# Optimization experiments

Measured on AMD Instinct MI355X. Metric: run time of the kernel, lower is better.

## Reference

```python
import jax, jax.numpy as jnp
import numpy as np

DIM = 1024
B, K = 8192, 16


def setup_inputs() -> dict:
    key = jax.random.key(0)
    ks = jax.random.split(key, 7)
    # xavier_uniform bound for square [C,C]: sqrt(6/(C+C))
    bq = float(np.sqrt(6.0 / (DIM + DIM)))
    ba_bound = float(np.sqrt(6.0 / (DIM + 1)))
    return {
        "query": jax.random.normal(ks[0], (B, DIM), dtype=jnp.float32),
        "key": jax.random.normal(ks[1], (B, K, DIM), dtype=jnp.float32),
        "value": jax.random.normal(ks[2], (B, K, DIM), dtype=jnp.float32),
        "Wq": jax.random.uniform(ks[3], (DIM, DIM), jnp.float32, -bq, bq),
        "Wk": jax.random.uniform(ks[4], (DIM, DIM), jnp.float32, -bq, bq),
        "Wa": jax.random.uniform(ks[5], (1, DIM), jnp.float32, -ba_bound, ba_bound),
        "ba": jnp.ones((1,), dtype=jnp.float32),
    }


def reference(query, key, value, Wq, Wk, Wa, ba):
    # query: [B, C]; key/value: [B, K, C]
    C = query.shape[-1]
    res = query
    q = query[:, None, :]                       # [B, 1, C]
    k = jnp.concatenate([q, key], axis=1)       # [B, K+1, C] (query prepended)
    v = jnp.concatenate([q, value], axis=1)     # [B, K+1, C]
    qp = q @ Wq.T                               # [B, 1, C]
    kp = k @ Wk.T                               # [B, K+1, C]
    scale = 1.0 / jnp.sqrt(jnp.asarray(C, dtype=jnp.float32))
    scores = jnp.einsum('bqc,bkc->bqk', qp, kp) * scale   # [B, 1, K+1]
    attn_w = jax.nn.softmax(scores, axis=-1)
    attn = jnp.einsum('bqk,bkc->bqc', attn_w, v)[:, 0, :]  # [B, C]
    alpha = jax.nn.sigmoid(res @ Wa.T + ba)     # [B, 1]
    out = res + alpha * attn                    # gated residual
    # F.normalize(p=2, dim=-1, eps=1e-12)
    norm = jnp.linalg.norm(out, axis=-1, keepdims=True)
    return out / jnp.maximum(norm, 1e-12)
```

## Files before the change

### kernel.cpp

```cpp
#include <hip/hip_runtime.h>
#include <hip/hip_bf16.h>

#define DIM   1024
#define BATCH 8192
#define KV    16

typedef __attribute__((ext_vector_type(4))) float f32x4;
typedef __attribute__((ext_vector_type(8))) short short8;

static __device__ __forceinline__ unsigned short f2bf(float x) {
  return __builtin_bit_cast(unsigned short, __float2bfloat16(x));
}
static __device__ __forceinline__ float bf2f(unsigned short x) {
  return __bfloat162float(__builtin_bit_cast(__hip_bfloat16, x));
}
static __device__ __forceinline__ float dot4(f32x4 a, f32x4 b) {
  return a.x * b.x + a.y * b.y + a.z * b.z + a.w * b.w;
}

static __device__ __forceinline__ void gl_lds16(const unsigned short* g, unsigned short* l) {
  __builtin_amdgcn_global_load_lds(
      (const __attribute__((address_space(1))) void*)g,
      (__attribute__((address_space(3))) void*)l, 16, 0, 0);
}

__global__ __launch_bounds__(256) void prep(const float* __restrict__ query,
                                            unsigned short* __restrict__ qbf,
                                            const float* __restrict__ Wq,
                                            const float* __restrict__ Wk,
                                            unsigned short* __restrict__ WqT,
                                            unsigned short* __restrict__ WkT) {
  if (blockIdx.z == 2) {
    int bid = blockIdx.y * 32 + blockIdx.x;
    int i = bid * 256 + threadIdx.x;
    const f32x4* in = (const f32x4*)query;
    ushort4* out = (ushort4*)qbf;
    #pragma unroll
    for (int r = 0; r < 8; ++r) {
      int idx = i + r * 262144;
      f32x4 f = in[idx];
      ushort4 o;
      o.x = f2bf(f.x); o.y = f2bf(f.y); o.z = f2bf(f.z); o.w = f2bf(f.w);
      out[idx] = o;
    }
  } else {
    __shared__ float tile[32][33];
    const float* src = blockIdx.z ? Wk : Wq;
    unsigned short* dst = blockIdx.z ? WkT : WqT;
    int tx = threadIdx.x & 31, ty = threadIdx.x >> 5;
    int x = blockIdx.x * 32 + tx;
    int y0 = blockIdx.y * 32;
    #pragma unroll
    for (int i = ty; i < 32; i += 8)
      tile[i][tx] = src[(size_t)(y0 + i) * DIM + x];
    __syncthreads();
    int x2 = blockIdx.y * 32 + tx;
    int y2 = blockIdx.x * 32;
    #pragma unroll
    for (int i = ty; i < 32; i += 8)
      dst[(size_t)(y2 + i) * DIM + x2] = f2bf(tile[tx][i]);
  }
}

__global__ __launch_bounds__(256) void gemm_nt64(const unsigned short* __restrict__ A,
                                                 const unsigned short* __restrict__ B,
                                                 unsigned short* __restrict__ C,
                                                 int N, int K) {
  __shared__ __align__(16) unsigned short As[64 * 32];
  __shared__ __align__(16) unsigned short Bs[64 * 32];
  const int tid = threadIdx.x;
  const int lane = tid & 63;
  const int wave = tid >> 6;
  const int wr = wave >> 1, wc = wave & 1;
  const size_t bm = (size_t)blockIdx.x * 64;
  const size_t bn = (size_t)blockIdx.y * 64;

  f32x4 acc[2][2];
  #pragma unroll
  for (int m = 0; m < 2; ++m)
    #pragma unroll
    for (int n = 0; n < 2; ++n)
      acc[m][n] = (f32x4){0.f, 0.f, 0.f, 0.f};

  const int r0 = tid >> 2;
  const int cc = (tid & 3) * 8;
  const int kg = lane >> 4;
  const int rowf = lane & 15;

  for (int kt = 0; kt < K; kt += 32) {
    gl_lds16(A + (bm + r0) * K + kt + cc, As + tid * 8);
    gl_lds16(B + (bn + r0) * K + kt + cc, Bs + tid * 8);
    __syncthreads();
    short8 af[2], bfr[2];
    #pragma unroll
    for (int m = 0; m < 2; ++m)
      af[m] = *(const short8*)(As + ((wr * 32 + m * 16 + rowf) * 32 + kg * 8));
    #pragma unroll
    for (int n = 0; n < 2; ++n)
      bfr[n] = *(const short8*)(Bs + ((wc * 32 + n * 16 + rowf) * 32 + kg * 8));
    #pragma unroll
    for (int m = 0; m < 2; ++m)
      #pragma unroll
      for (int n = 0; n < 2; ++n)
        acc[m][n] = __builtin_amdgcn_mfma_f32_16x16x32_bf16(af[m], bfr[n], acc[m][n], 0, 0, 0);
    __syncthreads();
  }

  const int rq = (lane >> 4) * 4;
  const int colf = lane & 15;
  #pragma unroll
  for (int m = 0; m < 2; ++m)
    #pragma unroll
    for (int n = 0; n < 2; ++n)
      #pragma unroll
      for (int i = 0; i < 4; ++i)
        C[(bm + wr * 32 + m * 16 + rq + i) * N + bn + wc * 32 + n * 16 + colf] =
            f2bf(acc[m][n][i]);
}

__global__ __launch_bounds__(256) void gemm_u(const unsigned short* __restrict__ A,
                                              const unsigned short* __restrict__ B,
                                              unsigned short* __restrict__ C,
                                              int ntN, int ldc) {
  __shared__ __align__(16) unsigned short As[128 * 64];
  __shared__ __align__(16) unsigned short Bs[128 * 64];

  const int cpx = gridDim.x >> 3;
  const int wg = (blockIdx.x & 7) * cpx + (blockIdx.x >> 3);
  const size_t bm = (size_t)(wg / ntN) * 128;
  const size_t bn = (size_t)(wg % ntN) * 128;

  const int tid = threadIdx.x;
  const int lane = tid & 63;
  const int wave = tid >> 6;
  const int wr = wave >> 1, wc = wave & 1;

  f32x4 acc[4][4];
  #pragma unroll
  for (int m = 0; m < 4; ++m)
    #pragma unroll
    for (int n = 0; n < 4; ++n)
      acc[m][n] = (f32x4){0.f, 0.f, 0.f, 0.f};

  const int kg = lane >> 4;
  const int rowf = lane & 15;

  for (int kt = 0; kt < DIM; kt += 64) {
    #pragma unroll
    for (int it = 0; it < 4; ++it) {
      int c = it * 256 + tid;
      int r = c >> 3;
      int ko = (c & 7) * 8;
      gl_lds16(A + (bm + r) * DIM + kt + ko, As + c * 8);
      gl_lds16(B + (bn + r) * DIM + kt + ko, Bs + c * 8);
    }
    __syncthreads();
    #pragma unroll
    for (int ks = 0; ks < 2; ++ks) {
      short8 af[4], bfr[4];
      #pragma unroll
      for (int m = 0; m < 4; ++m)
        af[m] = *(const short8*)(As + (wr * 64 + m * 16 + rowf) * 64 + ks * 32 + kg * 8);
      #pragma unroll
      for (int n = 0; n < 4; ++n)
        bfr[n] = *(const short8*)(Bs + (wc * 64 + n * 16 + rowf) * 64 + ks * 32 + kg * 8);
      #pragma unroll
      for (int m = 0; m < 4; ++m)
        #pragma unroll
        for (int n = 0; n < 4; ++n)
          acc[m][n] = __builtin_amdgcn_mfma_f32_16x16x32_bf16(af[m], bfr[n], acc[m][n], 0, 0, 0);
    }
    __syncthreads();
  }

  const int rq = (lane >> 4) * 4;
  const int colf = lane & 15;
  #pragma unroll
  for (int m = 0; m < 4; ++m)
    #pragma unroll
    for (int n = 0; n < 4; ++n)
      #pragma unroll
      for (int i = 0; i < 4; ++i) {
        size_t row = bm + wr * 64 + m * 16 + rq + i;
        size_t col = bn + wc * 64 + n * 16 + colf;
        C[row * (size_t)ldc + col] = f2bf(acc[m][n][i]);
      }
}

__global__ __launch_bounds__(256) void epilogue(const unsigned short* __restrict__ qbf,
                                                const float* __restrict__ key,
                                                const float* __restrict__ value,
                                                const float* __restrict__ Wa,
                                                const float* __restrict__ ba,
                                                const unsigned short* __restrict__ u,
                                                float* __restrict__ out) {
  const int b = blockIdx.x;
  const int tid = threadIdx.x;
  const int lane = tid & 63, wave = tid >> 6;
  const f32x4* k4 = (const f32x4*)(key + (size_t)b * KV * DIM);
  const f32x4* v4 = (const f32x4*)(value + (size_t)b * KV * DIM);

  ushort4 qb4 = *(const ushort4*)(qbf + (size_t)b * DIM + tid * 4);
  f32x4 qv;
  qv.x = bf2f(qb4.x); qv.y = bf2f(qb4.y); qv.z = bf2f(qb4.z); qv.w = bf2f(qb4.w);
  ushort4 ub = ((const ushort4*)(u + (size_t)b * 2048))[tid];
  f32x4 uv;
  uv.x = bf2f(ub.x); uv.y = bf2f(ub.y); uv.z = bf2f(ub.z); uv.w = bf2f(ub.w);
  f32x4 wv = ((const f32x4*)Wa)[tid];

  float s[17];
  s[0] = dot4(qv, uv);
  float ad = dot4(qv, wv);
  #pragma unroll
  for (int j = 1; j <= 16; ++j) {
    f32x4 kv = __builtin_nontemporal_load(k4 + (j - 1) * 256 + tid);
    s[j] = dot4(uv, kv);
  }

  f32x4 vv[16];
  #pragma unroll
  for (int j = 0; j < 16; ++j)
    vv[j] = __builtin_nontemporal_load(v4 + j * 256 + tid);

  #pragma unroll
  for (int m = 32; m >= 1; m >>= 1) {
    #pragma unroll
    for (int j = 0; j < 17; ++j) s[j] += __shfl_xor(s[j], m);
    ad += __shfl_xor(ad, m);
  }
  __shared__ float red[4][18];
  if (lane == 0) {
    #pragma unroll
    for (int j = 0; j < 17; ++j) red[wave][j] = s[j];
    red[wave][17] = ad;
  }
  __syncthreads();

  float wt[17];
  float mx = -1e30f;
  #pragma unroll
  for (int j = 0; j < 17; ++j) {
    float t = (red[0][j] + red[1][j] + red[2][j] + red[3][j]) * 0.03125f;
    wt[j] = t;
    mx = fmaxf(mx, t);
  }
  float den = 0.f;
  #pragma unroll
  for (int j = 0; j < 17; ++j) {
    wt[j] = expf(wt[j] - mx);
    den += wt[j];
  }
  float adt = red[0][17] + red[1][17] + red[2][17] + red[3][17] + ba[0];
  float alpha = 1.0f / (1.0f + expf(-adt));
  float am = alpha / den;

  f32x4 acc = qv * wt[0];
  #pragma unroll
  for (int j = 1; j <= 16; ++j) acc += vv[j - 1] * wt[j];
  f32x4 t = qv + acc * am;

  float ssp = dot4(t, t);
  #pragma unroll
  for (int m = 32; m >= 1; m >>= 1) ssp += __shfl_xor(ssp, m);
  __shared__ float red2[4];
  if (lane == 0) red2[wave] = ssp;
  __syncthreads();
  float nrm = sqrtf(red2[0] + red2[1] + red2[2] + red2[3]);
  float inv = 1.0f / fmaxf(nrm, 1e-12f);

  __builtin_nontemporal_store(t * inv, (f32x4*)(out + (size_t)b * DIM) + tid);
}

extern "C" void kernel_launch(void* const* d_in, const int* in_sizes, int n_in,
                              void* d_out, int out_size, void* d_ws, size_t ws_size,
                              hipStream_t stream) {
  const float* query = (const float*)d_in[0];
  const float* key   = (const float*)d_in[1];
  const float* value = (const float*)d_in[2];
  const float* Wq    = (const float*)d_in[3];
  const float* Wk    = (const float*)d_in[4];
  const float* Wa    = (const float*)d_in[5];
  const float* ba    = (const float*)d_in[6];

  unsigned short* qbf = (unsigned short*)d_ws;
  unsigned short* WqT = qbf + (size_t)BATCH * DIM;
  unsigned short* WkT = WqT + (size_t)DIM * DIM;
  unsigned short* Mt  = WkT + (size_t)DIM * DIM;
  unsigned short* ubf = (unsigned short*)d_out;

  prep<<<dim3(32, 32, 3), 256, 0, stream>>>(query, qbf, Wq, Wk, WqT, WkT);
  gemm_nt64<<<dim3(16, 16), 256, 0, stream>>>(WkT, WqT, Mt, DIM, DIM);
  gemm_u<<<512, 256, 0, stream>>>(qbf, Mt, ubf, DIM / 128, 2048);
  epilogue<<<BATCH, 256, 0, stream>>>(qbf, key, value, Wa, ba, ubf, (float*)d_out);
}
```

Baseline: 246.2 us.

## Fuse query bf16 conversion into GEMM A-tile load and drop qbf buffer

Removes the separate query-to-bf16 pass from the prep kernel. gemm_u now reads fp32 query directly, converts it to bf16 in registers and stores it to LDS, with the K tile shrunk from 64 to 32. The epilogue reads fp32 query directly. This saves a 32MB read and 16MB write pass plus the qbf buffer. In exchange, gemm_u reads twice the A bytes and each A-tile load becomes a synchronous register round-trip instead of an async global-to-LDS copy. The smaller K step also doubles the number of barriers per GEMM.

```diff
diff --git a/kernel.cpp b/kernel.cpp
--- a/kernel.cpp
+++ b/kernel.cpp
@@ -24,42 +24,25 @@
       (__attribute__((address_space(3))) void*)l, 16, 0, 0);
 }
 
-__global__ __launch_bounds__(256) void prep(const float* __restrict__ query,
-                                            unsigned short* __restrict__ qbf,
-                                            const float* __restrict__ Wq,
-                                            const float* __restrict__ Wk,
-                                            unsigned short* __restrict__ WqT,
-                                            unsigned short* __restrict__ WkT) {
-  if (blockIdx.z == 2) {
-    int bid = blockIdx.y * 32 + blockIdx.x;
-    int i = bid * 256 + threadIdx.x;
-    const f32x4* in = (const f32x4*)query;
-    ushort4* out = (ushort4*)qbf;
-    #pragma unroll
-    for (int r = 0; r < 8; ++r) {
-      int idx = i + r * 262144;
-      f32x4 f = in[idx];
-      ushort4 o;
-      o.x = f2bf(f.x); o.y = f2bf(f.y); o.z = f2bf(f.z); o.w = f2bf(f.w);
-      out[idx] = o;
-    }
-  } else {
-    __shared__ float tile[32][33];
-    const float* src = blockIdx.z ? Wk : Wq;
-    unsigned short* dst = blockIdx.z ? WkT : WqT;
-    int tx = threadIdx.x & 31, ty = threadIdx.x >> 5;
-    int x = blockIdx.x * 32 + tx;
-    int y0 = blockIdx.y * 32;
-    #pragma unroll
-    for (int i = ty; i < 32; i += 8)
-      tile[i][tx] = src[(size_t)(y0 + i) * DIM + x];
-    __syncthreads();
-    int x2 = blockIdx.y * 32 + tx;
-    int y2 = blockIdx.x * 32;
-    #pragma unroll
-    for (int i = ty; i < 32; i += 8)
-      dst[(size_t)(y2 + i) * DIM + x2] = f2bf(tile[tx][i]);
-  }
+__global__ __launch_bounds__(256) void transpose_w(const float* __restrict__ Wq,
+                                                   const float* __restrict__ Wk,
+                                                   unsigned short* __restrict__ WqT,
+                                                   unsigned short* __restrict__ WkT) {
+  __shared__ float tile[32][33];
+  const float* src = blockIdx.z ? Wk : Wq;
+  unsigned short* dst = blockIdx.z ? WkT : WqT;
+  int tx = threadIdx.x & 31, ty = threadIdx.x >> 5;
+  int x = blockIdx.x * 32 + tx;
+  int y0 = blockIdx.y * 32;
+  #pragma unroll
+  for (int i = ty; i < 32; i += 8)
+    tile[i][tx] = src[(size_t)(y0 + i) * DIM + x];
+  __syncthreads();
+  int x2 = blockIdx.y * 32 + tx;
+  int y2 = blockIdx.x * 32;
+  #pragma unroll
+  for (int i = ty; i < 32; i += 8)
+    dst[(size_t)(y2 + i) * DIM + x2] = f2bf(tile[tx][i]);
 }
 
 __global__ __launch_bounds__(256) void gemm_nt64(const unsigned short* __restrict__ A,
@@ -118,12 +101,12 @@
             f2bf(acc[m][n][i]);
 }
 
-__global__ __launch_bounds__(256) void gemm_u(const unsigned short* __restrict__ A,
+__global__ __launch_bounds__(256) void gemm_u(const float* __restrict__ Af,
                                               const unsigned short* __restrict__ B,
                                               unsigned short* __restrict__ C,
                                               int ntN, int ldc) {
-  __shared__ __align__(16) unsigned short As[128 * 64];
-  __shared__ __align__(16) unsigned short Bs[128 * 64];
+  __shared__ __align__(16) unsigned short As[128 * 32];
+  __shared__ __align__(16) unsigned short Bs[128 * 32];
 
   const int cpx = gridDim.x >> 3;
   const int wg = (blockIdx.x & 7) * cpx + (blockIdx.x >> 3);
@@ -144,32 +127,35 @@
 
   const int kg = lane >> 4;
   const int rowf = lane & 15;
-
-  for (int kt = 0; kt < DIM; kt += 64) {
+  const int br0 = tid >> 2;
+  const int bcc = (tid & 3) * 8;
+
+  for (int kt = 0; kt < DIM; kt += 32) {
+    gl_lds16(B + (bn + br0) * DIM + kt + bcc, Bs + tid * 8);
+    gl_lds16(B + (bn + 64 + br0) * DIM + kt + bcc, Bs + 2048 + tid * 8);
     #pragma unroll
     for (int it = 0; it < 4; ++it) {
       int c = it * 256 + tid;
       int r = c >> 3;
-      int ko = (c & 7) * 8;
-      gl_lds16(A + (bm + r) * DIM + kt + ko, As + c * 8);
-      gl_lds16(B + (bn + r) * DIM + kt + ko, Bs + c * 8);
+      int ko = (c & 7) * 4;
+      f32x4 f = *(const f32x4*)(Af + (bm + r) * DIM + kt + ko);
+      ushort4 o;
+      o.x = f2bf(f.x); o.y = f2bf(f.y); o.z = f2bf(f.z); o.w = f2bf(f.w);
+      *(ushort4*)(As + r * 32 + ko) = o;
     }
     __syncthreads();
-    #pragma unroll
-    for (int ks = 0; ks < 2; ++ks) {
-      short8 af[4], bfr[4];
-      #pragma unroll
-      for (int m = 0; m < 4; ++m)
-        af[m] = *(const short8*)(As + (wr * 64 + m * 16 + rowf) * 64 + ks * 32 + kg * 8);
+    short8 af[4], bfr[4];
+    #pragma unroll
+    for (int m = 0; m < 4; ++m)
+      af[m] = *(const short8*)(As + ((wr * 64 + m * 16 + rowf) * 32 + kg * 8));
+    #pragma unroll
+    for (int n = 0; n < 4; ++n)
+      bfr[n] = *(const short8*)(Bs + ((wc * 64 + n * 16 + rowf) * 32 + kg * 8));
+    #pragma unroll
+    for (int m = 0; m < 4; ++m)
       #pragma unroll
       for (int n = 0; n < 4; ++n)
-        bfr[n] = *(const short8*)(Bs + (wc * 64 + n * 16 + rowf) * 64 + ks * 32 + kg * 8);
-      #pragma unroll
-      for (int m = 0; m < 4; ++m)
-        #pragma unroll
-        for (int n = 0; n < 4; ++n)
-          acc[m][n] = __builtin_amdgcn_mfma_f32_16x16x32_bf16(af[m], bfr[n], acc[m][n], 0, 0, 0);
-    }
+        acc[m][n] = __builtin_amdgcn_mfma_f32_16x16x32_bf16(af[m], bfr[n], acc[m][n], 0, 0, 0);
     __syncthreads();
   }
 
@@ -187,7 +173,7 @@
       }
 }
 
-__global__ __launch_bounds__(256) void epilogue(const unsigned short* __restrict__ qbf,
+__global__ __launch_bounds__(256) void epilogue(const float* __restrict__ query,
                                                 const float* __restrict__ key,
                                                 const float* __restrict__ value,
                                                 const float* __restrict__ Wa,
@@ -200,9 +186,7 @@
   const f32x4* k4 = (const f32x4*)(key + (size_t)b * KV * DIM);
   const f32x4* v4 = (const f32x4*)(value + (size_t)b * KV * DIM);
 
-  ushort4 qb4 = *(const ushort4*)(qbf + (size_t)b * DIM + tid * 4);
-  f32x4 qv;
-  qv.x = bf2f(qb4.x); qv.y = bf2f(qb4.y); qv.z = bf2f(qb4.z); qv.w = bf2f(qb4.w);
+  f32x4 qv = ((const f32x4*)(query + (size_t)b * DIM))[tid];
   ushort4 ub = ((const ushort4*)(u + (size_t)b * 2048))[tid];
   f32x4 uv;
   uv.x = bf2f(ub.x); uv.y = bf2f(ub.y); uv.z = bf2f(ub.z); uv.w = bf2f(ub.w);
@@ -282,14 +266,13 @@
   const float* Wa    = (const float*)d_in[5];
   const float* ba    = (const float*)d_in[6];
 
-  unsigned short* qbf = (unsigned short*)d_ws;
-  unsigned short* WqT = qbf + (size_t)BATCH * DIM;
+  unsigned short* WqT = (unsigned short*)d_ws;
   unsigned short* WkT = WqT + (size_t)DIM * DIM;
   unsigned short* Mt  = WkT + (size_t)DIM * DIM;
   unsigned short* ubf = (unsigned short*)d_out;
 
-  prep<<<dim3(32, 32, 3), 256, 0, stream>>>(query, qbf, Wq, Wk, WqT, WkT);
+  transpose_w<<<dim3(32, 32, 2), 256, 0, stream>>>(Wq, Wk, WqT, WkT);
   gemm_nt64<<<dim3(16, 16), 256, 0, stream>>>(WkT, WqT, Mt, DIM, DIM);
-  gemm_u<<<512, 256, 0, stream>>>(qbf, Mt, ubf, DIM / 128, 2048);
-  epilogue<<<BATCH, 256, 0, stream>>>(qbf, key, value, Wa, ba, ubf, (float*)d_out);
-}
+  gemm_u<<<512, 256, 0, stream>>>(query, Mt, ubf, DIM / 128, 2048);
+  epilogue<<<BATCH, 256, 0, stream>>>(query, key, value, Wa, ba, ubf, (float*)d_out);
+}
```

New measurement: 244.3 us. About the same (-0.7%).
